# Performance work log

Measured on AMD Instinct MI355X. Metric: run time of the kernel, lower is better.

Reference implementation:

```python
import jax, jax.numpy as jnp
import numpy as np

SIMPLE_W = 1.0
NON_SIMPLE_W = 5.0

# connectivity offset sets (exclude center)
_ALL26 = [(a, b, c) for a in (-1, 0, 1) for b in (-1, 0, 1) for c in (-1, 0, 1) if (a, b, c) != (0, 0, 0)]
OFF6 = [o for o in _ALL26 if abs(o[0]) + abs(o[1]) + abs(o[2]) == 1]          # scipy default structure
OFF18 = [o for o in _ALL26 if not (abs(o[0]) == 1 and abs(o[1]) == 1 and abs(o[2]) == 1)]  # the 's' structure
OFF26 = _ALL26                                                                  # np.ones((3,3,3))


def global_label(fg):
    """Connected-component labels (6-connectivity) via max-propagation.
    Labels are distinct positive ints per component (values differ from scipy's
    1..K but only label *equality* is used downstream). fg: bool [D,H,W]."""
    D, H, W = fg.shape
    idx = (jnp.arange(fg.size, dtype=jnp.int32) + 1).reshape(fg.shape)
    lab0 = jnp.where(fg, idx, 0)

    def step(lab):
        p = jnp.pad(lab, 1)
        m = lab
        for dz, dy, dx in OFF6:
            m = jnp.maximum(m, p[1 + dz:1 + dz + D, 1 + dy:1 + dy + H, 1 + dx:1 + dx + W])
        return jnp.where(fg, m, 0)

    def cond(c):
        return ~c[1]

    def body(c):
        lab, _ = c
        new = step(lab)
        return new, jnp.all(new == lab)

    lab, _ = jax.lax.while_loop(cond, body, (lab0, jnp.array(False)))
    return lab


def local_ncomp(mask, offsets):
    """Number of connected components inside each 3x3x3 window.
    mask: bool [N,3,3,3]. Max-propagation of unique seeds for 26 iters
    (>= max path length among 27 voxels); a component is counted where the
    surviving max label equals its own seed."""
    seed = (jnp.arange(27, dtype=jnp.int32) + 1).reshape(3, 3, 3)
    lab0 = jnp.where(mask, seed, 0)

    def body(_, lab):
        p = jnp.pad(lab, ((0, 0), (1, 1), (1, 1), (1, 1)))
        m = lab
        for dz, dy, dx in offsets:
            m = jnp.maximum(m, p[:, 1 + dz:4 + dz, 1 + dy:4 + dy, 1 + dx:4 + dx])
        return jnp.where(mask, m, 0)

    lab = jax.lax.fori_loop(0, 26, body, lab0)
    return jnp.sum((lab == seed) & mask, axis=(1, 2, 3))


def nonsimple_map(x):
    """Per-voxel non-simple-point indicator, float, same shape as x."""
    D, H, W = x.shape
    fg = x > 0
    glab = global_label(fg)
    p = jnp.pad(glab, 1, mode='edge')  # np.pad(..., 'edge')
    # 3x3x3 label windows per voxel -> [N,3,3,3]
    wins = jnp.stack([p[dz:dz + D, dy:dy + H, dx:dx + W]
                      for dz in range(3) for dy in range(3) for dx in range(3)], axis=-1)
    wins = wins.reshape(-1, 3, 3, 3)
    center = wins[:, 1, 1, 1]  # [N]
    c = center[:, None, None, None]
    # test 1: complement-of-center-label components (18-connectivity) must be exactly 1
    n1 = local_ncomp(wins != c, OFF18)
    # test 2: center-label components with center voxel removed (26-conn) must be exactly 1
    mask2 = (wins == c).at[:, 1, 1, 1].set(False)
    n2 = local_ncomp(mask2, OFF26)
    ns = (center != 0) & ((n1 != 1) | (n2 != 1))
    return ns.reshape(D, H, W).astype(x.dtype)


def setup_inputs() -> dict:
    key = jax.random.key(0)
    k1, k2 = jax.random.split(key)
    D = H = W = 64
    prediction = jax.random.normal(k1, (D, H, W), dtype=jnp.float32)
    label = jax.random.randint(k2, (D, H, W), 0, 2).astype(jnp.float32)
    return {"prediction": prediction, "label": label}


def reference(prediction, label):
    pw = nonsimple_map(prediction)
    lw = nonsimple_map(label)
    w_bool = (pw + lw) > 0
    weight = jnp.where(w_bool, NON_SIMPLE_W, SIMPLE_W).astype(prediction.dtype)
    # BCEWithLogitsLoss(reduction='none'): max(x,0) - x*y + log(1+exp(-|x|))
    cost = jnp.maximum(prediction, 0.0) - prediction * label + jnp.log1p(jnp.exp(-jnp.abs(prediction)))
    return jnp.mean(weight * cost)
```

## Files before the change

kernel.cpp:

```cpp
#include <hip/hip_runtime.h>

#define DIM 64
#define NVOX (DIM * DIM * DIM)
#define EPF 53248

__device__ __forceinline__ int find_root_link(int* L, int v) {
    for (;;) {
        int p = L[v];
        if (p == v) return v;
        int gp = L[p];
        if (gp == p) return p;
        L[v] = gp;
        v = gp;
    }
}

__device__ __forceinline__ void unite(int* L, int a, int b) {
    int ra = find_root_link(L, a);
    int rb = find_root_link(L, b);
    while (ra != rb) {
        if (ra > rb) { int t = ra; ra = rb; rb = t; }
        int old = atomicCAS(&L[rb], rb, ra);
        if (old == rb) break;
        rb = find_root_link(L, old);
        ra = find_root_link(L, ra);
    }
}

__device__ __forceinline__ int chase(const int* __restrict__ L, int p) {
    int q = L[p];
    while (q != p) { p = q; q = L[p]; }
    return p;
}

__global__ __launch_bounds__(512)
void local_ccl(const float* __restrict__ pred,
               const float* __restrict__ lab,
               int* __restrict__ LP, int* __restrict__ LL,
               float* __restrict__ out) {
    __shared__ int s_lab[2048];
    int t = threadIdx.x;
    if (blockIdx.x == 0 && blockIdx.y == 0 && t == 0) *out = 0.0f;
    int b = blockIdx.x;
    int tx = b & 3, ty = (b >> 2) & 3, tz = b >> 4;
    int X0 = tx << 4, Y0 = ty << 4, Z0 = tz << 3;

    const float* src = blockIdx.y ? lab : pred;
    int* Lg = blockIdx.y ? LL : LP;

    int l0 = t << 2;
    int v0 = ((Z0 + (l0 >> 8)) << 12) | ((Y0 + ((l0 >> 4) & 15)) << 6)
           | (X0 + (l0 & 15));

    unsigned nib;
    {
        const float4 f = *reinterpret_cast<const float4*>(src + v0);
        nib  = (unsigned)(f.x > 0.0f);
        nib |= (unsigned)(f.y > 0.0f) << 1;
        nib |= (unsigned)(f.z > 0.0f) << 2;
        nib |= (unsigned)(f.w > 0.0f) << 3;
    }

    unsigned rm = nib << ((t & 3) << 2);
    rm |= __shfl_xor(rm, 1, 64);
    rm |= __shfl_xor(rm, 2, 64);

    int rowbase = l0 & ~15;
    int xbase = l0 & 15;

    {
        int4 s;
        int lbl[4];
#pragma unroll
        for (int k = 0; k < 4; ++k) {
            int xpos = xbase + k;
            unsigned u = ~rm & ((1u << xpos) - 1u);
            int start = u ? (32 - __clz(u)) : 0;
            lbl[k] = ((nib >> k) & 1) ? rowbase + start : -1;
        }
        s.x = lbl[0]; s.y = lbl[1]; s.z = lbl[2]; s.w = lbl[3];
        *reinterpret_cast<int4*>(&s_lab[l0]) = s;
    }
    __syncthreads();

    {
        int py_a = -2, py_b = -2;
        int pz_a = -2, pz_b = -2;
#pragma unroll
        for (int k = 0; k < 4; ++k) {
            if (!((nib >> k) & 1)) continue;
            int l = l0 + k;
            int a = s_lab[l];
            int ly = (l >> 4) & 15, lz = l >> 8;
            if (ly < 15) {
                int nb = s_lab[l + 16];
                if (nb >= 0 && !(a == py_a && nb == py_b)) {
                    unite(s_lab, a, nb);
                    py_a = a; py_b = nb;
                }
            }
            if (lz < 7) {
                int nb = s_lab[l + 256];
                if (nb >= 0 && !(a == pz_a && nb == pz_b)) {
                    unite(s_lab, a, nb);
                    pz_a = a; pz_b = nb;
                }
            }
        }
    }
    __syncthreads();

    {
        int rr[4];
#pragma unroll
        for (int k = 0; k < 4; ++k) {
            int g = -1;
            if ((nib >> k) & 1) {
                int p = s_lab[l0 + k];
                while (s_lab[p] != p) p = s_lab[p];
                g = ((Z0 + (p >> 8)) << 12) | ((Y0 + ((p >> 4) & 15)) << 6)
                  | (X0 + (p & 15));
            }
            rr[k] = g;
        }
        *reinterpret_cast<int4*>(Lg + v0) = make_int4(rr[0], rr[1], rr[2], rr[3]);
    }
}

__global__ __launch_bounds__(256)
void boundary_link(int* __restrict__ LP, int* __restrict__ LL) {
    int r = blockIdx.x * blockDim.x + threadIdx.x;
    int* L = blockIdx.y ? LL : LP;

    int v, n;
    if (r < 12288) {
        int plane = 15 + ((r >> 12) << 4);
        int ij = r & 4095;
        v = ((ij >> 6) << 12) | ((ij & 63) << 6) | plane;
        n = v + 1;
    } else if (r < 24576) {
        int r2 = r - 12288;
        int plane = 15 + ((r2 >> 12) << 4);
        int ij = r2 & 4095;
        v = ((ij >> 6) << 12) | (plane << 6) | (ij & 63);
        n = v + 64;
    } else {
        int r3 = r - 24576;
        int plane = 7 + ((r3 >> 12) << 3);
        int ij = r3 & 4095;
        v = (plane << 12) | ((ij >> 6) << 6) | (ij & 63);
        n = v + 4096;
    }

    int lane = threadIdx.x & 63;

    int pa = L[v], pb = L[n];
    bool go = (pa >= 0) & (pb >= 0);

    int xpa = __shfl_up(pa, 1, 64), xpb = __shfl_up(pb, 1, 64);
    if (lane && xpa == pa && xpb == pb) go = false;

    int r0 = -1, r1 = -1;
    if (go) {
        int u0 = chase(L, pa), u1 = chase(L, pb);
        r0 = min(u0, u1); r1 = max(u0, u1);
    }

    int q0 = __shfl_up(r0, 1, 64), q1 = __shfl_up(r1, 1, 64);
    bool dup = lane && (q0 == r0) && (q1 == r1);

    if (r0 >= 0 && r0 != r1 && !dup) unite(L, r0, r1);
}

__global__ __launch_bounds__(256)
void flatten(int* __restrict__ LP, int* __restrict__ LL) {
    int idx = blockIdx.x * blockDim.x + threadIdx.x;
    int* L = (idx < NVOX) ? LP : LL;
    int i = idx & (NVOX - 1);
    int p = L[i];
    if (p >= 0) {
        int r = chase(L, p);
        if (r != p) L[i] = r;
    }
}

#define MX_L 0x6DB6DB6u
#define MX_R 0x36DB6DBu
#define MY_L 0x7E3F1F8u
#define MY_R 0x0FC7E3Fu
#define M27  0x7FFFFFFu

__device__ __forceinline__ unsigned dil26(unsigned m) {
    m |= ((m << 1) & MX_L) | ((m >> 1) & MX_R);
    m |= ((m << 3) & MY_L) | ((m >> 3) & MY_R);
    m |= ((m << 9) & M27)  | (m >> 9);
    return m;
}
__device__ __forceinline__ unsigned dil18(unsigned m) {
    unsigned ax = m | ((m << 1) & MX_L) | ((m >> 1) & MX_R);
    unsigned ay = m | ((m << 3) & MY_L) | ((m >> 3) & MY_R);
    unsigned dxy = ax | ((ax << 3) & MY_L) | ((ax >> 3) & MY_R);
    unsigned dxz = ax | ((ax << 9) & M27)  | (ax >> 9);
    unsigned dyz = ay | ((ay << 9) & M27)  | (ay >> 9);
    return dxy | dxz | dyz;
}

__device__ __forceinline__ bool single18(unsigned m) {
    if (!m) return false;
    unsigned c = m & (~m + 1u);
    for (;;) {
        unsigned n = dil18(c) & m;
        if (n == m) return true;
        if (n == c) return false;
        c = n;
    }
}
__device__ __forceinline__ bool single26(unsigned m) {
    if (!m) return false;
    unsigned c = m & (~m + 1u);
    for (;;) {
        unsigned n = dil26(c) & m;
        if (n == m) return true;
        if (n == c) return false;
        c = n;
    }
}

#define HV2 600

__global__ __launch_bounds__(256, 4)
void finalize_kernel(const float* __restrict__ pred,
                     const float* __restrict__ lab,
                     const int* __restrict__ LP,
                     const int* __restrict__ LL,
                     float* __restrict__ out) {
    __shared__ int sP[HV2], sL[HV2];
    __shared__ float s_part[4];
    int t = threadIdx.x;
    int b = blockIdx.x;
    int rx = b & 7, ry = (b >> 3) & 7, rz = b >> 6;
    int x0 = rx << 3, y0 = ry << 3, z0 = rz << 2;

    int pv[3], lv[3];
#pragma unroll
    for (int j = 0; j < 3; ++j) {
        int i = t + (j << 8);
        if (i < HV2) {
            int hx = i % 10, rr = i / 10, hy = rr % 10, hz = rr / 10;
            int gx = x0 + hx - 1; gx = gx < 0 ? 0 : (gx > 63 ? 63 : gx);
            int gy = y0 + hy - 1; gy = gy < 0 ? 0 : (gy > 63 ? 63 : gy);
            int gz = z0 + hz - 1; gz = gz < 0 ? 0 : (gz > 63 ? 63 : gz);
            int gv = (gz << 12) | (gy << 6) | gx;
            pv[j] = LP[gv];
            lv[j] = LL[gv];
        }
    }
#pragma unroll
    for (int j = 0; j < 3; ++j) {
        int i = t + (j << 8);
        if (i < HV2) {
            sP[i] = pv[j];
            sL[i] = lv[j];
        }
    }
    __syncthreads();

    float acc;
    {
        int l = t;
        int lx = l & 7, ly = (l >> 3) & 7, lz = l >> 6;
        int x = x0 | lx, y = y0 | ly, z = z0 | lz;
        int v = (z << 12) | (y << 6) | x;
        int base = lz * 100 + ly * 10 + lx;

        bool nsP = false, nsL = false;
        {
            int c = sP[base + 111];
            if (c >= 0) {
                unsigned m1 = 0, m2 = 0; int k = 0;
#pragma unroll
                for (int kz = 0; kz < 3; ++kz)
#pragma unroll
                    for (int ky = 0; ky < 3; ++ky)
#pragma unroll
                        for (int kx = 0; kx < 3; ++kx, ++k) {
                            int w = sP[base + kz * 100 + ky * 10 + kx];
                            m1 |= (unsigned)(w != c) << k;
                            m2 |= (unsigned)(w == c) << k;
                        }
                m2 &= ~(1u << 13);
                nsP = !(single18(m1) && single26(m2));
            }
        }
        {
            int c = sL[base + 111];
            if (c >= 0) {
                unsigned m1 = 0, m2 = 0; int k = 0;
#pragma unroll
                for (int kz = 0; kz < 3; ++kz)
#pragma unroll
                    for (int ky = 0; ky < 3; ++ky)
#pragma unroll
                        for (int kx = 0; kx < 3; ++kx, ++k) {
                            int w = sL[base + kz * 100 + ky * 10 + kx];
                            m1 |= (unsigned)(w != c) << k;
                            m2 |= (unsigned)(w == c) << k;
                        }
                m2 &= ~(1u << 13);
                nsL = !(single18(m1) && single26(m2));
            }
        }

        float p = pred[v], lvf = lab[v];
        float cost = fmaxf(p, 0.0f) - p * lvf + log1pf(__expf(-fabsf(p)));
        acc = ((nsP || nsL) ? 5.0f : 1.0f) * cost;
    }

#pragma unroll
    for (int off = 32; off > 0; off >>= 1)
        acc += __shfl_down(acc, off, 64);
    if ((t & 63) == 0) s_part[t >> 6] = acc;
    __syncthreads();
    if (t == 0) {
        float s = s_part[0] + s_part[1] + s_part[2] + s_part[3];
        atomicAdd(out, s * (1.0f / (float)NVOX));
    }
}

extern "C" void kernel_launch(void* const* d_in, const int* in_sizes, int n_in,
                              void* d_out, int out_size, void* d_ws, size_t ws_size,
                              hipStream_t stream) {
    const float* pred = (const float*)d_in[0];
    const float* lab  = (const float*)d_in[1];
    float* out = (float*)d_out;

    int* LP = (int*)d_ws;
    int* LL = LP + NVOX;

    hipLaunchKernelGGL(local_ccl, dim3(128, 2), dim3(512), 0, stream,
                       pred, lab, LP, LL, out);
    hipLaunchKernelGGL(boundary_link, dim3(EPF / 256, 2), dim3(256), 0, stream,
                       LP, LL);
    hipLaunchKernelGGL(flatten, dim3(2 * NVOX / 256), dim3(256), 0, stream,
                       LP, LL);
    hipLaunchKernelGGL(finalize_kernel, dim3(1024), dim3(256), 0, stream,
                       pred, lab, LP, LL, out);
}
```

Before: 104.2 us.

## Drop flatten kernel, resolve roots in finalize, use atomicMin union

Removes the separate flatten launch and instead chases each label to its root while loading the halo tile in the finalize kernel. It also swaps the CAS-based union, which compressed paths through find_root_link, for an atomicMin loop that walks parent links directly. This saves one kernel launch and a full pass over both label arrays. In exchange, overlapping halos mean the same pointer chains are chased many times across blocks, and without path compression those chains may be longer. A leftover dead assignment of `a` in local_ccl has no effect.

```diff
diff --git a/kernel.cpp b/kernel.cpp
--- a/kernel.cpp
+++ b/kernel.cpp
@@ -4,26 +4,13 @@
 #define NVOX (DIM * DIM * DIM)
 #define EPF 53248
 
-__device__ __forceinline__ int find_root_link(int* L, int v) {
-    for (;;) {
-        int p = L[v];
-        if (p == v) return v;
-        int gp = L[p];
-        if (gp == p) return p;
-        L[v] = gp;
-        v = gp;
-    }
-}
-
 __device__ __forceinline__ void unite(int* L, int a, int b) {
-    int ra = find_root_link(L, a);
-    int rb = find_root_link(L, b);
+    int ra = a, rb = b;
     while (ra != rb) {
         if (ra > rb) { int t = ra; ra = rb; rb = t; }
-        int old = atomicCAS(&L[rb], rb, ra);
-        if (old == rb) break;
-        rb = find_root_link(L, old);
-        ra = find_root_link(L, ra);
+        int old = atomicMin(&L[rb], ra);
+        if (old == rb || old == ra) break;
+        rb = old;
     }
 }
 
@@ -90,7 +77,8 @@
         for (int k = 0; k < 4; ++k) {
             if (!((nib >> k) & 1)) continue;
             int l = l0 + k;
-            int a = s_lab[l];
+            int a = s_lab[l0 + k] >= 0 ? (l0 + k, s_lab[l]) : -1;
+            a = s_lab[l];
             int ly = (l >> 4) & 15, lz = l >> 8;
             if (ly < 15) {
                 int nb = s_lab[l + 16];
@@ -172,18 +160,6 @@
     if (r0 >= 0 && r0 != r1 && !dup) unite(L, r0, r1);
 }
 
-__global__ __launch_bounds__(256)
-void flatten(int* __restrict__ LP, int* __restrict__ LL) {
-    int idx = blockIdx.x * blockDim.x + threadIdx.x;
-    int* L = (idx < NVOX) ? LP : LL;
-    int i = idx & (NVOX - 1);
-    int p = L[i];
-    if (p >= 0) {
-        int r = chase(L, p);
-        if (r != p) L[i] = r;
-    }
-}
-
 #define MX_L 0x6DB6DB6u
 #define MX_R 0x36DB6DBu
 #define MY_L 0x7E3F1F8u
@@ -259,8 +235,12 @@
     for (int j = 0; j < 3; ++j) {
         int i = t + (j << 8);
         if (i < HV2) {
-            sP[i] = pv[j];
-            sL[i] = lv[j];
+            int p = pv[j];
+            if (p >= 0) p = chase(LP, p);
+            sP[i] = p;
+            p = lv[j];
+            if (p >= 0) p = chase(LL, p);
+            sL[i] = p;
         }
     }
     __syncthreads();
@@ -341,8 +321,6 @@
                        pred, lab, LP, LL, out);
     hipLaunchKernelGGL(boundary_link, dim3(EPF / 256, 2), dim3(256), 0, stream,
                        LP, LL);
-    hipLaunchKernelGGL(flatten, dim3(2 * NVOX / 256), dim3(256), 0, stream,
-                       LP, LL);
     hipLaunchKernelGGL(finalize_kernel, dim3(1024), dim3(256), 0, stream,
                        pred, lab, LP, LL, out);
 }
```

New measurement: 103.3 us. About the same (-0.8%).
